# Performance work log

Measured on AMD Instinct MI355X. Metric: run time of the kernel, lower is better.

## Reference

```python
import jax, jax.numpy as jnp
import numpy as np

PERMS = ((0, 1, 2, 3), (2, 1, 3, 0), (3, 1, 0, 2))


def setup_inputs() -> dict:
    key = jax.random.key(0)
    ks = jax.random.split(key, 10)
    N_n1, F = 50000, 128
    N_imp = 100000
    H = 512
    h = jax.random.normal(ks[0], (N_n1, F), dtype=jnp.float32)
    idx = jax.random.randint(ks[1], (N_imp, 4), 0, N_n1, dtype=jnp.int64)
    s = 0.05
    W1 = jax.random.normal(ks[2], (4 * F, H), dtype=jnp.float32) * s
    b1 = jax.random.normal(ks[3], (H,), dtype=jnp.float32) * s
    W2 = jax.random.normal(ks[4], (H, H), dtype=jnp.float32) * s
    b2 = jax.random.normal(ks[5], (H,), dtype=jnp.float32) * s
    W3 = jax.random.normal(ks[6], (H, H), dtype=jnp.float32) * s
    b3 = jax.random.normal(ks[7], (H,), dtype=jnp.float32) * s
    Wo = jax.random.normal(ks[8], (H, 2), dtype=jnp.float32) * s
    bo = jax.random.normal(ks[9], (2,), dtype=jnp.float32) * s
    return {"h": h, "idx": idx, "W1": W1, "b1": b1, "W2": W2, "b2": b2,
            "W3": W3, "b3": b3, "Wo": Wo, "bo": bo}


def reference(h, idx, W1, b1, W2, b2, W3, b3, Wo, bo):
    # Message passing: copy_u + mean over exactly one edge per relation == gather.
    hi = h[idx]  # [N, 4, F]
    N = hi.shape[0]
    # Stack the 3 permutations of the 4 neighbor features: [3, N, 4F]
    x = jnp.stack([hi[:, jnp.array(p), :].reshape(N, -1) for p in PERMS], axis=0)
    # Shared MLP (config = [512, relu] x 3), broadcast over permutation axis.
    x = jax.nn.relu(x @ W1 + b1)
    x = jax.nn.relu(x @ W2 + b2)
    x = jax.nn.relu(x @ W3 + b3)
    pooled = jnp.sum(x, axis=0)  # Janossy sum over permutations: [N, 512]
    return pooled @ Wo + bo  # [N, 2]
```

## Files before the change

### kernel.cpp

```cpp
#include <hip/hip_runtime.h>
#include <stdint.h>
#include <stddef.h>


typedef __attribute__((ext_vector_type(8))) short short8;
typedef __attribute__((ext_vector_type(16))) float f32x16;
typedef __attribute__((ext_vector_type(4))) float floatv4;
typedef __attribute__((ext_vector_type(8))) unsigned short ushort8;

#define GLOAD_LDS16(g, l)                                                      \
  __builtin_amdgcn_global_load_lds(                                            \
      (const __attribute__((address_space(1))) void*)(g),                      \
      (__attribute__((address_space(3))) void*)(l), 16, 0, 0)

__device__ __forceinline__ unsigned short f2bf(float f) {
  unsigned int u = __float_as_uint(f);
  u += 0x7fffu + ((u >> 16) & 1u);
  return (unsigned short)(u >> 16);
}
__device__ __forceinline__ float bf2f(unsigned short s) {
  return __uint_as_float(((unsigned int)s) << 16);
}

#define NNODES 100000
#define MTOT   300000
#define HD     512
#define NH     50000
#define LSTR   152

__global__ __launch_bounds__(256) void prep_w(const float* __restrict__ W1,
                                              const float* __restrict__ W2,
                                              const float* __restrict__ W3,
                                              unsigned short* __restrict__ Wt) {
  int t = blockIdx.x * 256 + threadIdx.x;
  int layer = t >> 18;
  int r = t & 262143;
  int e = r & 7;
  int q16 = r >> 3;
  int s = q16 & 1023;
  int blk = q16 >> 10;
  int nb = blk >> 3, kt = blk & 7;
  int c = ((s >> 8) << 1) | ((s >> 5) & 1);
  int row = ((s >> 6) & 3) * 32 + (s & 31);
  int n = nb * 128 + row;
  int k = kt * 64 + c * 8 + e;
  const float* W = layer == 0 ? W1 : (layer == 1 ? W2 : W3);
  Wt[t] = f2bf(W[k * 512 + n]);
}

__global__ __launch_bounds__(256) void prep_hb(const float* __restrict__ h,
                                               unsigned short* __restrict__ hb) {
  int t = blockIdx.x * 256 + threadIdx.x;
  int v = t >> 4, c8 = (t & 15) * 8;
  const floatv4* hp = (const floatv4*)(h + (size_t)v * 128 + c8);
  floatv4 f0 = hp[0], f1 = hp[1];
  ushort8 o;
#pragma unroll
  for (int e = 0; e < 4; ++e) {
    o[e] = f2bf(f0[e]);
    o[4 + e] = f2bf(f1[e]);
  }
  *(ushort8*)(hb + (size_t)v * 128 + c8) = o;
}

__global__ __launch_bounds__(256) void init_out(float* __restrict__ out,
                                                const float* __restrict__ bo) {
  int t = blockIdx.x * 256 + threadIdx.x;
  if (t < 2 * NNODES) out[t] = bo[t & 1];
}

template <int GATHER, int FINAL>
__global__ __launch_bounds__(256, 4) void gemm_k(
    const unsigned short* __restrict__ A,
    const int* __restrict__ idx,
    const unsigned short* __restrict__ Wt,
    const float* __restrict__ bias,
    unsigned short* __restrict__ Xout,
    float* __restrict__ out, const float* __restrict__ Wo,
    int mchunk0) {
  __shared__ __align__(16) char smem[39936];
  char* sB = smem;
  char* sA = smem + 16384;
  int* sIdx = (int*)(smem + 32768);
  float* sWo = (float*)(smem + 38912);

  const int t = threadIdx.x;
  int bx = blockIdx.x;
  int xcd = bx & 7, tq = bx >> 3;
  int cbk = tq & 3;
  int rb = xcd + ((tq >> 2) << 3);
  int n0 = cbk * 128;
  int rb8 = rb * 8;
  int w = t >> 6, l = t & 63;
  int wmq = (w >> 1) * 2, wnq = (w & 1) * 2;
  int m32 = l & 31, half = l >> 5;
  int wm = wmq * 32;

  if (GATHER) {
    if (t < 128) {
      int m = mchunk0 + rb * 128 + t;
      unsigned um = (unsigned)m;
      unsigned n = um / 3u;
      int p = (int)(um - n * 3u);
      if (n >= NNODES) n = 0;
      const unsigned pk0 = 0x320u, pk1 = 0x111u, pk2 = 0x032u, pk3 = 0x203u;
      int sh = p * 4;
      sIdx[t * 4 + 0] = idx[n * 4 + ((pk0 >> sh) & 0xFu)];
      sIdx[t * 4 + 1] = idx[n * 4 + ((pk1 >> sh) & 0xFu)];
      sIdx[t * 4 + 2] = idx[n * 4 + ((pk2 >> sh) & 0xFu)];
      sIdx[t * 4 + 3] = idx[n * 4 + ((pk3 >> sh) & 0xFu)];
    }
    __syncthreads();
  }

  f32x16 acc[2][2];
#pragma unroll
  for (int i = 0; i < 2; ++i)
#pragma unroll
    for (int j = 0; j < 2; ++j)
#pragma unroll
      for (int r = 0; r < 16; ++r) acc[i][j][r] = 0.f;

  for (int kt = 0; kt < 8; ++kt) {
    short8 afr[4][2];
    if (!GATHER) {
      const unsigned short* ga = A + ((size_t)(rb8 + kt) * 1024) * 8;
#pragma unroll
      for (int ks = 0; ks < 4; ++ks)
#pragma unroll
        for (int i = 0; i < 2; ++i)
          afr[ks][i] = *(const short8*)(ga +
              (size_t)(ks * 256 + (wmq + i) * 64 + l) * 8);
    }
    {
      const unsigned short* gb = Wt + ((size_t)(cbk * 8 + kt) * 1024 + t) * 8;
#pragma unroll
      for (int i = 0; i < 4; ++i)
        GLOAD_LDS16(gb + (size_t)i * 2048, sB + (i * 256 + t) * 16);
    }
    if (GATHER) {
      int jblk = kt >> 1;
      int inner = (kt & 1) * 64;
#pragma unroll
      for (int i = 0; i < 4; ++i) {
        int s = i * 256 + t;
        int r = s >> 3;
        int cl = (s & 7) ^ (r & 7);
        int src = sIdx[r * 4 + jblk];
        GLOAD_LDS16(A + (size_t)src * 128 + inner + cl * 8, sA + s * 16);
      }
    }
    __syncthreads();
#pragma unroll
    for (int ks = 0; ks < 4; ++ks) {
      short8 bfr[2];
#pragma unroll
      for (int j = 0; j < 2; ++j)
        bfr[j] = *(const short8*)(sB + (ks * 256 + (wnq + j) * 64 + l) * 16);
      if (GATHER) {
        short8 ag[2];
        int cbp = ((ks << 1) + half) ^ (m32 & 7);
#pragma unroll
        for (int i = 0; i < 2; ++i)
          ag[i] = *(const short8*)(sA + (wm + i * 32 + m32) * 128 + cbp * 16);
#pragma unroll
        for (int i = 0; i < 2; ++i)
#pragma unroll
          for (int j = 0; j < 2; ++j)
            acc[i][j] = __builtin_amdgcn_mfma_f32_32x32x16_bf16(
                ag[i], bfr[j], acc[i][j], 0, 0, 0);
      } else {
#pragma unroll
        for (int i = 0; i < 2; ++i)
#pragma unroll
          for (int j = 0; j < 2; ++j)
            acc[i][j] = __builtin_amdgcn_mfma_f32_32x32x16_bf16(
                afr[ks][i], bfr[j], acc[i][j], 0, 0, 0);
      }
    }
    __syncthreads();
  }

  unsigned short* L = (unsigned short*)smem;
  if (FINAL && t < 256) sWo[t] = Wo[n0 * 2 + t];
#pragma unroll
  for (int i = 0; i < 2; ++i)
#pragma unroll
    for (int j = 0; j < 2; ++j) {
      int coll = wnq * 32 + j * 32 + m32;
      float bv = bias[n0 + coll];
#pragma unroll
      for (int r = 0; r < 16; ++r) {
        int rowl = wm + i * 32 + (r & 3) + 8 * (r >> 2) + 4 * half;
        float v = fmaxf(acc[i][j][r] + bv, 0.f);
        L[rowl * LSTR + coll] = f2bf(v);
      }
    }
  __syncthreads();

  if (!FINAL) {
#pragma unroll
    for (int v = 0; v < 8; ++v) {
      int chunk = v * 256 + t;
      int ktsel = chunk >> 10;
      int s = chunk & 1023;
      int ks_l = s >> 8;
      int rowhi = (s >> 6) & 3;
      int hb_ = (s >> 5) & 1;
      int row = rowhi * 32 + (s & 31);
      int col_local = ktsel * 64 + (((ks_l << 1) | hb_) << 3);
      ushort8 val = *(const ushort8*)(L + row * LSTR + col_local);
      *(ushort8*)(Xout + ((size_t)(rb8 + 2 * cbk + ktsel) * 1024 + s) * 8) = val;
    }
  } else {
    int r2 = t >> 1, jo = t & 1;
    int grow = mchunk0 + rb * 128 + r2;
    if (grow < MTOT) {
      const unsigned short* Lr = L + r2 * LSTR;
      float s = 0.f;
#pragma unroll
      for (int cc = 0; cc < 128; cc += 2) {
        unsigned int pair = *(const unsigned int*)(Lr + cc);
        s += bf2f((unsigned short)(pair & 0xffffu)) * sWo[2 * cc + jo];
        s += bf2f((unsigned short)(pair >> 16)) * sWo[2 * cc + 2 + jo];
      }
      int node = grow / 3;
      atomicAdd(out + node * 2 + jo, s);
    }
  }
}

extern "C" void kernel_launch(void* const* d_in, const int* in_sizes, int n_in,
                              void* d_out, int out_size, void* d_ws,
                              size_t ws_size, hipStream_t stream) {
  const float* h  = (const float*)d_in[0];
  const int*   ix = (const int*)d_in[1];
  const float* W1 = (const float*)d_in[2];
  const float* b1 = (const float*)d_in[3];
  const float* W2 = (const float*)d_in[4];
  const float* b2 = (const float*)d_in[5];
  const float* W3 = (const float*)d_in[6];
  const float* b3 = (const float*)d_in[7];
  const float* Wo = (const float*)d_in[8];
  const float* bo = (const float*)d_in[9];
  float* out = (float*)d_out;

  unsigned short* ws = (unsigned short*)d_ws;
  unsigned short* Wt = ws;
  unsigned short* hb = Wt + 786432;
  unsigned short* bufs = hb + 6400000;
  const size_t baseBytes = (786432ull + 6400000ull) * 2;

  size_t avail = ws_size > baseBytes ? ws_size - baseBytes : 0;
  size_t ncap = avail / (2ull * 3 * HD * sizeof(unsigned short));
  size_t nc = (ncap / 2048) * 2048;
  if (nc > 32768) nc = 32768;
  if (nc == 0) nc = 2048;
  unsigned short* X1 = bufs;
  unsigned short* X2 = X1 + nc * 3 * HD;

  prep_w<<<3072, 256, 0, stream>>>(W1, W2, W3, Wt);
  prep_hb<<<NH * 16 / 256, 256, 0, stream>>>(h, hb);
  init_out<<<(2 * NNODES + 255) / 256, 256, 0, stream>>>(out, bo);

  for (size_t n0c = 0; n0c < NNODES; n0c += nc) {
    size_t remn = (size_t)NNODES - n0c;
    size_t ncp = remn < nc ? ((remn + 2047) / 2048) * 2048 : nc;
    int rows = (int)(ncp * 3);
    int RB = rows / 128;
    int m0 = (int)(3 * n0c);
    gemm_k<1, 0><<<RB * 4, 256, 0, stream>>>(hb, ix, Wt, b1, X1, nullptr,
                                             nullptr, m0);
    gemm_k<0, 0><<<RB * 4, 256, 0, stream>>>(X1, nullptr, Wt + 262144, b2, X2,
                                             nullptr, nullptr, m0);
    gemm_k<0, 1><<<RB * 4, 256, 0, stream>>>(X2, nullptr, Wt + 524288, b3,
                                             nullptr, out, Wo, m0);
  }
}
```

Before: 666.4 us.

## Use 256x256 tiles with double-buffered LDS pipeline and 16x16x32 MFMA

Each GEMM block now computes a 256x256 output tile with 512 threads, instead of a 128x128 tile with 256 threads. Both A and B tiles are staged into double-buffered LDS with XOR-swizzled async global-to-LDS loads. The loads for the next k-steps are interleaved with four MFMA phases, separated by explicit barriers and setprio. Weight and intermediate activation layouts are rewritten to match the new tiling, and the epilogue is widened. This raises arithmetic intensity and overlaps memory with compute, at the cost of about 138KB of LDS per block, which limits occupancy to one block per CU, and more complex synchronisation.

```diff
diff --git a/kernel.cpp b/kernel.cpp
--- a/kernel.cpp
+++ b/kernel.cpp
@@ -4,7 +4,6 @@
 
 
 typedef __attribute__((ext_vector_type(8))) short short8;
-typedef __attribute__((ext_vector_type(16))) float f32x16;
 typedef __attribute__((ext_vector_type(4))) float floatv4;
 typedef __attribute__((ext_vector_type(8))) unsigned short ushort8;
 
@@ -26,7 +25,7 @@
 #define MTOT   300000
 #define HD     512
 #define NH     50000
-#define LSTR   152
+#define LSTR   264
 
 __global__ __launch_bounds__(256) void prep_w(const float* __restrict__ W1,
                                               const float* __restrict__ W2,
@@ -36,14 +35,12 @@
   int layer = t >> 18;
   int r = t & 262143;
   int e = r & 7;
-  int q16 = r >> 3;
-  int s = q16 & 1023;
-  int blk = q16 >> 10;
-  int nb = blk >> 3, kt = blk & 7;
-  int c = ((s >> 8) << 1) | ((s >> 5) & 1);
-  int row = ((s >> 6) & 3) * 32 + (s & 31);
-  int n = nb * 128 + row;
-  int k = kt * 64 + c * 8 + e;
+  int g = (r >> 3) & 7;
+  int row = (r >> 6) & 255;
+  int cbkt = r >> 14;
+  int cb = cbkt >> 3, kt = cbkt & 7;
+  int n = cb * 256 + row;
+  int k = kt * 64 + g * 8 + e;
   const float* W = layer == 0 ? W1 : (layer == 1 ? W2 : W3);
   Wt[t] = f2bf(W[k * 512 + n]);
 }
@@ -69,8 +66,77 @@
   if (t < 2 * NNODES) out[t] = bo[t & 1];
 }
 
+
+#define BAR()                            \
+  __builtin_amdgcn_sched_barrier(0);     \
+  __builtin_amdgcn_s_barrier();          \
+  __builtin_amdgcn_sched_barrier(0)
+
+#define STAGE_A(kk, odd)                                                       \
+  {                                                                            \
+    char* db = smem + ((kk) & 1) * 32768;                                      \
+    _Pragma("unroll")                                                          \
+    for (int qq = 0; qq < 2; ++qq) {                                           \
+      int q = (odd) + qq * 2;                                                  \
+      int row = q * 64 + tr;                                                   \
+      const unsigned short* sp;                                                \
+      if (GATHER) {                                                            \
+        int srcn = sIdx[row * 4 + ((kk) >> 1)];                                \
+        sp = A + (size_t)srcn * 128 + ((kk) & 1) * 64 + sxg * 8;               \
+      } else {                                                                 \
+        sp = A + (((size_t)(rb * 8 + (kk)) * 256 + row) * 8 + sxg) * 8;        \
+      }                                                                        \
+      GLOAD_LDS16(sp, db + q * 8192 + t * 16);                                 \
+    }                                                                          \
+  }
+
+#define STAGE_B(kk, odd)                                                       \
+  {                                                                            \
+    char* db = smem + 65536 + ((kk) & 1) * 32768;                              \
+    _Pragma("unroll")                                                          \
+    for (int qq = 0; qq < 2; ++qq) {                                           \
+      int q = (odd) + qq * 2;                                                  \
+      const unsigned short* sp =                                               \
+          Wt + (((size_t)(cb * 8 + (kk)) * 256 + q * 64 + tr) * 8 + sxg) * 8;  \
+      GLOAD_LDS16(sp, db + q * 8192 + t * 16);                                 \
+    }                                                                          \
+  }
+
+#define LDA(mh)                                                                \
+  _Pragma("unroll")                                                            \
+  for (int mi = 0; mi < 4; ++mi) {                                             \
+    const char* rbase = bA + (wmbase + (mh) * 64 + mi * 16 + lr) * 128;        \
+    a[mi][0] = *(const short8*)(rbase + xb0);                                  \
+    a[mi][1] = *(const short8*)(rbase + xb1);                                  \
+  }
+
+#define LDB(nh)                                                                \
+  _Pragma("unroll")                                                            \
+  for (int nj = 0; nj < 2; ++nj) {                                             \
+    const char* rbase = bB + (wnbase + (nh) * 32 + nj * 16 + lr) * 128;        \
+    b[(nh) * 2 + nj][0] = *(const short8*)(rbase + xb0);                       \
+    b[(nh) * 2 + nj][1] = *(const short8*)(rbase + xb1);                       \
+  }
+
+#define MMA(mh, nh)                                                            \
+  __builtin_amdgcn_s_setprio(1);                                               \
+  _Pragma("unroll")                                                            \
+  for (int mi = 0; mi < 4; ++mi)                                               \
+    _Pragma("unroll")                                                          \
+    for (int nj = 0; nj < 2; ++nj) {                                           \
+      acc[(mh) * 4 + mi][(nh) * 2 + nj] =                                      \
+          __builtin_amdgcn_mfma_f32_16x16x32_bf16(                             \
+              a[mi][0], b[(nh) * 2 + nj][0],                                   \
+              acc[(mh) * 4 + mi][(nh) * 2 + nj], 0, 0, 0);                     \
+      acc[(mh) * 4 + mi][(nh) * 2 + nj] =                                      \
+          __builtin_amdgcn_mfma_f32_16x16x32_bf16(                             \
+              a[mi][1], b[(nh) * 2 + nj][1],                                   \
+              acc[(mh) * 4 + mi][(nh) * 2 + nj], 0, 0, 0);                     \
+    }                                                                          \
+  __builtin_amdgcn_s_setprio(0);
+
 template <int GATHER, int FINAL>
-__global__ __launch_bounds__(256, 4) void gemm_k(
+__global__ __launch_bounds__(512, 2) void gemm_k(
     const unsigned short* __restrict__ A,
     const int* __restrict__ idx,
     const unsigned short* __restrict__ Wt,
@@ -78,31 +144,36 @@
     unsigned short* __restrict__ Xout,
     float* __restrict__ out, const float* __restrict__ Wo,
     int mchunk0) {
-  __shared__ __align__(16) char smem[39936];
-  char* sB = smem;
-  char* sA = smem + 16384;
-  int* sIdx = (int*)(smem + 32768);
-  float* sWo = (float*)(smem + 38912);
+  __shared__ __align__(16) char smem[141312];
+  int* sIdx = (int*)(smem + 135168);
+  float* sWo = (float*)(smem + 139264);
 
   const int t = threadIdx.x;
   int bx = blockIdx.x;
-  int xcd = bx & 7, tq = bx >> 3;
-  int cbk = tq & 3;
-  int rb = xcd + ((tq >> 2) << 3);
-  int n0 = cbk * 128;
-  int rb8 = rb * 8;
-  int w = t >> 6, l = t & 63;
-  int wmq = (w >> 1) * 2, wnq = (w & 1) * 2;
-  int m32 = l & 31, half = l >> 5;
-  int wm = wmq * 32;
-
+  int cpx = (int)gridDim.x >> 3;
+  int wg = (bx & 7) * cpx + (bx >> 3);
+  int cb = wg & 1;
+  int rb = wg >> 1;
+  int n0 = cb * 256;
+
+  const int l = t & 63;
+  const int w = t >> 6;
+  const int wmbase = (w >> 2) * 128;
+  const int wnbase = (w & 3) * 64;
+  const int lr = l & 15, lk = l >> 4;
+  const int xb0 = (lk ^ (lr & 7)) * 16;
+  const int xb1 = xb0 ^ 64;
+  const int tr = t >> 3;
+  const int sxg = (t & 7) ^ (tr & 7);
+
+  if (FINAL) sWo[t] = Wo[n0 * 2 + t];
   if (GATHER) {
-    if (t < 128) {
-      int m = mchunk0 + rb * 128 + t;
+    if (t < 256) {
+      int m = mchunk0 + rb * 256 + t;
       unsigned um = (unsigned)m;
       unsigned n = um / 3u;
       int p = (int)(um - n * 3u);
-      if (n >= NNODES) n = 0;
+      if (n >= (unsigned)NNODES) n = 0;
       const unsigned pk0 = 0x320u, pk1 = 0x111u, pk2 = 0x032u, pk3 = 0x203u;
       int sh = p * 4;
       sIdx[t * 4 + 0] = idx[n * 4 + ((pk0 >> sh) & 0xFu)];
@@ -113,113 +184,91 @@
     __syncthreads();
   }
 
-  f32x16 acc[2][2];
-#pragma unroll
-  for (int i = 0; i < 2; ++i)
-#pragma unroll
-    for (int j = 0; j < 2; ++j)
-#pragma unroll
-      for (int r = 0; r < 16; ++r) acc[i][j][r] = 0.f;
-
-  for (int kt = 0; kt < 8; ++kt) {
-    short8 afr[4][2];
-    if (!GATHER) {
-      const unsigned short* ga = A + ((size_t)(rb8 + kt) * 1024) * 8;
-#pragma unroll
-      for (int ks = 0; ks < 4; ++ks)
-#pragma unroll
-        for (int i = 0; i < 2; ++i)
-          afr[ks][i] = *(const short8*)(ga +
-              (size_t)(ks * 256 + (wmq + i) * 64 + l) * 8);
+  floatv4 acc[8][4];
+#pragma unroll
+  for (int i = 0; i < 8; ++i)
+#pragma unroll
+    for (int j = 0; j < 4; ++j)
+#pragma unroll
+      for (int r = 0; r < 4; ++r) acc[i][j][r] = 0.f;
+
+  STAGE_A(0, 0); STAGE_A(0, 1); STAGE_B(0, 0); STAGE_B(0, 1);
+  STAGE_A(1, 0); STAGE_B(1, 0); STAGE_B(1, 1);
+  asm volatile("s_waitcnt vmcnt(6)" ::: "memory");
+  BAR();
+
+#pragma unroll 2
+  for (int k = 0; k < 8; ++k) {
+    const char* bA = smem + (k & 1) * 32768;
+    const char* bB = smem + 65536 + (k & 1) * 32768;
+    short8 a[4][2], b[4][2];
+    LDA(0);
+    LDB(0);
+    if (k < 7) STAGE_A(k + 1, 1);
+    BAR();
+    MMA(0, 0);
+    BAR();
+    LDB(1);
+    if (k < 6) STAGE_A(k + 2, 0);
+    BAR();
+    MMA(0, 1);
+    BAR();
+    LDA(1);
+    if (k < 6) STAGE_B(k + 2, 0);
+    BAR();
+    MMA(1, 0);
+    BAR();
+    if (k < 6) STAGE_B(k + 2, 1);
+    BAR();
+    MMA(1, 1);
+    if (k < 6) {
+      asm volatile("s_waitcnt vmcnt(6)" ::: "memory");
+    } else {
+      asm volatile("s_waitcnt vmcnt(0)" ::: "memory");
     }
-    {
-      const unsigned short* gb = Wt + ((size_t)(cbk * 8 + kt) * 1024 + t) * 8;
-#pragma unroll
-      for (int i = 0; i < 4; ++i)
-        GLOAD_LDS16(gb + (size_t)i * 2048, sB + (i * 256 + t) * 16);
-    }
-    if (GATHER) {
-      int jblk = kt >> 1;
-      int inner = (kt & 1) * 64;
-#pragma unroll
-      for (int i = 0; i < 4; ++i) {
-        int s = i * 256 + t;
-        int r = s >> 3;
-        int cl = (s & 7) ^ (r & 7);
-        int src = sIdx[r * 4 + jblk];
-        GLOAD_LDS16(A + (size_t)src * 128 + inner + cl * 8, sA + s * 16);
+    BAR();
+  }
+
+  unsigned short* L = (unsigned short*)smem;
+  {
+    float bv[4];
+#pragma unroll
+    for (int nj = 0; nj < 4; ++nj) bv[nj] = bias[n0 + wnbase + nj * 16 + lr];
+#pragma unroll
+    for (int mi = 0; mi < 8; ++mi)
+#pragma unroll
+      for (int nj = 0; nj < 4; ++nj) {
+        int col = wnbase + nj * 16 + lr;
+#pragma unroll
+        for (int r = 0; r < 4; ++r) {
+          int row = wmbase + mi * 16 + lk * 4 + r;
+          float v = fmaxf(acc[mi][nj][r] + bv[nj], 0.f);
+          L[row * LSTR + col] = f2bf(v);
+        }
       }
-    }
-    __syncthreads();
-#pragma unroll
-    for (int ks = 0; ks < 4; ++ks) {
-      short8 bfr[2];
-#pragma unroll
-      for (int j = 0; j < 2; ++j)
-        bfr[j] = *(const short8*)(sB + (ks * 256 + (wnq + j) * 64 + l) * 16);
-      if (GATHER) {
-        short8 ag[2];
-        int cbp = ((ks << 1) + half) ^ (m32 & 7);
-#pragma unroll
-        for (int i = 0; i < 2; ++i)
-          ag[i] = *(const short8*)(sA + (wm + i * 32 + m32) * 128 + cbp * 16);
-#pragma unroll
-        for (int i = 0; i < 2; ++i)
-#pragma unroll
-          for (int j = 0; j < 2; ++j)
-            acc[i][j] = __builtin_amdgcn_mfma_f32_32x32x16_bf16(
-                ag[i], bfr[j], acc[i][j], 0, 0, 0);
-      } else {
-#pragma unroll
-        for (int i = 0; i < 2; ++i)
-#pragma unroll
-          for (int j = 0; j < 2; ++j)
-            acc[i][j] = __builtin_amdgcn_mfma_f32_32x32x16_bf16(
-                afr[ks][i], bfr[j], acc[i][j], 0, 0, 0);
-      }
-    }
-    __syncthreads();
-  }
-
-  unsigned short* L = (unsigned short*)smem;
-  if (FINAL && t < 256) sWo[t] = Wo[n0 * 2 + t];
-#pragma unroll
-  for (int i = 0; i < 2; ++i)
-#pragma unroll
-    for (int j = 0; j < 2; ++j) {
-      int coll = wnq * 32 + j * 32 + m32;
-      float bv = bias[n0 + coll];
-#pragma unroll
-      for (int r = 0; r < 16; ++r) {
-        int rowl = wm + i * 32 + (r & 3) + 8 * (r >> 2) + 4 * half;
-        float v = fmaxf(acc[i][j][r] + bv, 0.f);
-        L[rowl * LSTR + coll] = f2bf(v);
-      }
-    }
+  }
   __syncthreads();
 
   if (!FINAL) {
 #pragma unroll
-    for (int v = 0; v < 8; ++v) {
-      int chunk = v * 256 + t;
-      int ktsel = chunk >> 10;
-      int s = chunk & 1023;
-      int ks_l = s >> 8;
-      int rowhi = (s >> 6) & 3;
-      int hb_ = (s >> 5) & 1;
-      int row = rowhi * 32 + (s & 31);
-      int col_local = ktsel * 64 + (((ks_l << 1) | hb_) << 3);
-      ushort8 val = *(const ushort8*)(L + row * LSTR + col_local);
-      *(ushort8*)(Xout + ((size_t)(rb8 + 2 * cbk + ktsel) * 1024 + s) * 8) = val;
+    for (int it = 0; it < 16; ++it) {
+      int slot = it * 512 + t;
+      int ktq = slot >> 11;
+      int s = slot & 2047;
+      int row = s >> 3, g = s & 7;
+      ushort8 val = *(const ushort8*)(L + row * LSTR + ktq * 64 + g * 8);
+      *(ushort8*)(Xout +
+                  ((size_t)((rb * 8 + cb * 4 + ktq) * 256 + row) * 8 + g) * 8) =
+          val;
     }
   } else {
     int r2 = t >> 1, jo = t & 1;
-    int grow = mchunk0 + rb * 128 + r2;
+    int grow = mchunk0 + rb * 256 + r2;
     if (grow < MTOT) {
       const unsigned short* Lr = L + r2 * LSTR;
       float s = 0.f;
 #pragma unroll
-      for (int cc = 0; cc < 128; cc += 2) {
+      for (int cc = 0; cc < 256; cc += 2) {
         unsigned int pair = *(const unsigned int*)(Lr + cc);
         s += bf2f((unsigned short)(pair & 0xffffu)) * sWo[2 * cc + jo];
         s += bf2f((unsigned short)(pair >> 16)) * sWo[2 * cc + 2 + jo];
@@ -267,13 +316,13 @@
     size_t remn = (size_t)NNODES - n0c;
     size_t ncp = remn < nc ? ((remn + 2047) / 2048) * 2048 : nc;
     int rows = (int)(ncp * 3);
-    int RB = rows / 128;
+    int RB = rows / 256;
     int m0 = (int)(3 * n0c);
-    gemm_k<1, 0><<<RB * 4, 256, 0, stream>>>(hb, ix, Wt, b1, X1, nullptr,
+    gemm_k<1, 0><<<RB * 2, 512, 0, stream>>>(hb, ix, Wt, b1, X1, nullptr,
                                              nullptr, m0);
-    gemm_k<0, 0><<<RB * 4, 256, 0, stream>>>(X1, nullptr, Wt + 262144, b2, X2,
+    gemm_k<0, 0><<<RB * 2, 512, 0, stream>>>(X1, nullptr, Wt + 262144, b2, X2,
                                              nullptr, nullptr, m0);
-    gemm_k<0, 1><<<RB * 4, 256, 0, stream>>>(X2, nullptr, Wt + 524288, b3,
+    gemm_k<0, 1><<<RB * 2, 512, 0, stream>>>(X2, nullptr, Wt + 524288, b3,
                                              nullptr, out, Wo, m0);
   }
 }
```

After: 750.7 us. 12.7% more time.

## Split gather GEMM from dense GEMMs and double M-tile for dense layers

Applied to the files above, without the earlier changes.

Separates the gather-based first layer into its own kernel and gives layers 2 and 3 a new kernel with 256-row M tiles (4x2 MFMA tiles per wave), halving the number of blocks that reload each weight tile. The intermediate activation layout is changed to 256-row blocks so each wave loads its A fragments directly from global memory. The larger tile raises register pressure (launch bounds lowered to 2 blocks per SM) and the epilogue is done in two halves through a smaller LDS buffer, with extra barriers.

```diff
diff --git a/kernel.cpp b/kernel.cpp
--- a/kernel.cpp
+++ b/kernel.cpp
@@ -27,6 +27,7 @@
 #define HD     512
 #define NH     50000
 #define LSTR   152
+#define LSTR2  136
 
 __global__ __launch_bounds__(256) void prep_w(const float* __restrict__ W1,
                                               const float* __restrict__ W2,
@@ -69,20 +70,18 @@
   if (t < 2 * NNODES) out[t] = bo[t & 1];
 }
 
-template <int GATHER, int FINAL>
-__global__ __launch_bounds__(256, 4) void gemm_k(
+
+__global__ __launch_bounds__(256, 4) void gemm_g(
     const unsigned short* __restrict__ A,
     const int* __restrict__ idx,
     const unsigned short* __restrict__ Wt,
     const float* __restrict__ bias,
     unsigned short* __restrict__ Xout,
-    float* __restrict__ out, const float* __restrict__ Wo,
     int mchunk0) {
   __shared__ __align__(16) char smem[39936];
   char* sB = smem;
   char* sA = smem + 16384;
   int* sIdx = (int*)(smem + 32768);
-  float* sWo = (float*)(smem + 38912);
 
   const int t = threadIdx.x;
   int bx = blockIdx.x;
@@ -90,28 +89,25 @@
   int cbk = tq & 3;
   int rb = xcd + ((tq >> 2) << 3);
   int n0 = cbk * 128;
-  int rb8 = rb * 8;
   int w = t >> 6, l = t & 63;
   int wmq = (w >> 1) * 2, wnq = (w & 1) * 2;
   int m32 = l & 31, half = l >> 5;
   int wm = wmq * 32;
 
-  if (GATHER) {
-    if (t < 128) {
-      int m = mchunk0 + rb * 128 + t;
-      unsigned um = (unsigned)m;
-      unsigned n = um / 3u;
-      int p = (int)(um - n * 3u);
-      if (n >= NNODES) n = 0;
-      const unsigned pk0 = 0x320u, pk1 = 0x111u, pk2 = 0x032u, pk3 = 0x203u;
-      int sh = p * 4;
-      sIdx[t * 4 + 0] = idx[n * 4 + ((pk0 >> sh) & 0xFu)];
-      sIdx[t * 4 + 1] = idx[n * 4 + ((pk1 >> sh) & 0xFu)];
-      sIdx[t * 4 + 2] = idx[n * 4 + ((pk2 >> sh) & 0xFu)];
-      sIdx[t * 4 + 3] = idx[n * 4 + ((pk3 >> sh) & 0xFu)];
-    }
-    __syncthreads();
-  }
+  if (t < 128) {
+    int m = mchunk0 + rb * 128 + t;
+    unsigned um = (unsigned)m;
+    unsigned n = um / 3u;
+    int p = (int)(um - n * 3u);
+    if (n >= NNODES) n = 0;
+    const unsigned pk0 = 0x320u, pk1 = 0x111u, pk2 = 0x032u, pk3 = 0x203u;
+    int sh = p * 4;
+    sIdx[t * 4 + 0] = idx[n * 4 + ((pk0 >> sh) & 0xFu)];
+    sIdx[t * 4 + 1] = idx[n * 4 + ((pk1 >> sh) & 0xFu)];
+    sIdx[t * 4 + 2] = idx[n * 4 + ((pk2 >> sh) & 0xFu)];
+    sIdx[t * 4 + 3] = idx[n * 4 + ((pk3 >> sh) & 0xFu)];
+  }
+  __syncthreads();
 
   f32x16 acc[2][2];
 #pragma unroll
@@ -122,23 +118,13 @@
       for (int r = 0; r < 16; ++r) acc[i][j][r] = 0.f;
 
   for (int kt = 0; kt < 8; ++kt) {
-    short8 afr[4][2];
-    if (!GATHER) {
-      const unsigned short* ga = A + ((size_t)(rb8 + kt) * 1024) * 8;
-#pragma unroll
-      for (int ks = 0; ks < 4; ++ks)
-#pragma unroll
-        for (int i = 0; i < 2; ++i)
-          afr[ks][i] = *(const short8*)(ga +
-              (size_t)(ks * 256 + (wmq + i) * 64 + l) * 8);
-    }
     {
       const unsigned short* gb = Wt + ((size_t)(cbk * 8 + kt) * 1024 + t) * 8;
 #pragma unroll
       for (int i = 0; i < 4; ++i)
         GLOAD_LDS16(gb + (size_t)i * 2048, sB + (i * 256 + t) * 16);
     }
-    if (GATHER) {
+    {
       int jblk = kt >> 1;
       int inner = (kt & 1) * 64;
 #pragma unroll
@@ -157,32 +143,22 @@
 #pragma unroll
       for (int j = 0; j < 2; ++j)
         bfr[j] = *(const short8*)(sB + (ks * 256 + (wnq + j) * 64 + l) * 16);
-      if (GATHER) {
-        short8 ag[2];
-        int cbp = ((ks << 1) + half) ^ (m32 & 7);
-#pragma unroll
-        for (int i = 0; i < 2; ++i)
-          ag[i] = *(const short8*)(sA + (wm + i * 32 + m32) * 128 + cbp * 16);
-#pragma unroll
-        for (int i = 0; i < 2; ++i)
-#pragma unroll
-          for (int j = 0; j < 2; ++j)
-            acc[i][j] = __builtin_amdgcn_mfma_f32_32x32x16_bf16(
-                ag[i], bfr[j], acc[i][j], 0, 0, 0);
-      } else {
-#pragma unroll
-        for (int i = 0; i < 2; ++i)
-#pragma unroll
-          for (int j = 0; j < 2; ++j)
-            acc[i][j] = __builtin_amdgcn_mfma_f32_32x32x16_bf16(
-                afr[ks][i], bfr[j], acc[i][j], 0, 0, 0);
-      }
+      short8 ag[2];
+      int cbp = ((ks << 1) + half) ^ (m32 & 7);
+#pragma unroll
+      for (int i = 0; i < 2; ++i)
+        ag[i] = *(const short8*)(sA + (wm + i * 32 + m32) * 128 + cbp * 16);
+#pragma unroll
+      for (int i = 0; i < 2; ++i)
+#pragma unroll
+        for (int j = 0; j < 2; ++j)
+          acc[i][j] = __builtin_amdgcn_mfma_f32_32x32x16_bf16(
+              ag[i], bfr[j], acc[i][j], 0, 0, 0);
     }
     __syncthreads();
   }
 
   unsigned short* L = (unsigned short*)smem;
-  if (FINAL && t < 256) sWo[t] = Wo[n0 * 2 + t];
 #pragma unroll
   for (int i = 0; i < 2; ++i)
 #pragma unroll
@@ -198,35 +174,135 @@
     }
   __syncthreads();
 
-  if (!FINAL) {
-#pragma unroll
-    for (int v = 0; v < 8; ++v) {
-      int chunk = v * 256 + t;
-      int ktsel = chunk >> 10;
-      int s = chunk & 1023;
-      int ks_l = s >> 8;
-      int rowhi = (s >> 6) & 3;
-      int hb_ = (s >> 5) & 1;
-      int row = rowhi * 32 + (s & 31);
-      int col_local = ktsel * 64 + (((ks_l << 1) | hb_) << 3);
-      ushort8 val = *(const ushort8*)(L + row * LSTR + col_local);
-      *(ushort8*)(Xout + ((size_t)(rb8 + 2 * cbk + ktsel) * 1024 + s) * 8) = val;
-    }
-  } else {
-    int r2 = t >> 1, jo = t & 1;
-    int grow = mchunk0 + rb * 128 + r2;
-    if (grow < MTOT) {
-      const unsigned short* Lr = L + r2 * LSTR;
-      float s = 0.f;
-#pragma unroll
-      for (int cc = 0; cc < 128; cc += 2) {
-        unsigned int pair = *(const unsigned int*)(Lr + cc);
-        s += bf2f((unsigned short)(pair & 0xffffu)) * sWo[2 * cc + jo];
-        s += bf2f((unsigned short)(pair >> 16)) * sWo[2 * cc + 2 + jo];
+  int mblk = rb >> 1, rhalf = (rb & 1) * 4;
+#pragma unroll
+  for (int it = 0; it < 8; ++it) {
+    int c = it * 256 + t;
+    int ktl = c >> 10;
+    int s = c & 1023;
+    int ks = s >> 8, rg = (s >> 6) & 3, hf = (s >> 5) & 1, m = s & 31;
+    ushort8 val =
+        *(const ushort8*)(L + (rg * 32 + m) * LSTR + ktl * 64 + (ks * 2 + hf) * 8);
+    *(ushort8*)(Xout + ((size_t)((mblk * 8 + cbk * 2 + ktl) * 2048) + ks * 512 +
+                        (rhalf + rg) * 64 + hf * 32 + m) * 8) = val;
+  }
+}
+
+template <int FINAL>
+__global__ __launch_bounds__(256, 2) void gemm_d(
+    const unsigned short* __restrict__ A,
+    const unsigned short* __restrict__ Wt,
+    const float* __restrict__ bias,
+    unsigned short* __restrict__ Xout,
+    float* __restrict__ out, const float* __restrict__ Wo,
+    int mchunk0) {
+  __shared__ __align__(16) char smem[36864];
+  char* sB = smem;
+  float* sWo = (float*)(smem + 35840);
+
+  const int t = threadIdx.x;
+  int bx = blockIdx.x;
+  int xcd = bx & 7, tq = bx >> 3;
+  int cbk = tq & 3;
+  int rb = xcd + ((tq >> 2) << 3);
+  int n0 = cbk * 128;
+  int w = t >> 6, l = t & 63;
+  int wr = w >> 1, wc = w & 1;
+  int wm32 = wr * 4;
+  int m32 = l & 31, half = l >> 5;
+
+  if (FINAL) sWo[t] = Wo[n0 * 2 + t];
+
+  f32x16 acc[4][2];
+#pragma unroll
+  for (int i = 0; i < 4; ++i)
+#pragma unroll
+    for (int j = 0; j < 2; ++j)
+#pragma unroll
+      for (int r = 0; r < 16; ++r) acc[i][j][r] = 0.f;
+
+  for (int kt = 0; kt < 8; ++kt) {
+    short8 afr[4][4];
+    const unsigned short* ga = A + (size_t)(rb * 8 + kt) * 16384;
+#pragma unroll
+    for (int ks = 0; ks < 4; ++ks)
+#pragma unroll
+      for (int mi = 0; mi < 4; ++mi)
+        afr[ks][mi] = *(const short8*)(ga +
+            (size_t)(ks * 512 + (wm32 + mi) * 64 + l) * 8);
+    {
+      const unsigned short* gb = Wt + ((size_t)(cbk * 8 + kt) * 1024 + t) * 8;
+#pragma unroll
+      for (int i = 0; i < 4; ++i)
+        GLOAD_LDS16(gb + (size_t)i * 2048, sB + (i * 256 + t) * 16);
+    }
+    __syncthreads();
+#pragma unroll
+    for (int ks = 0; ks < 4; ++ks) {
+      short8 bfr[2];
+#pragma unroll
+      for (int j = 0; j < 2; ++j)
+        bfr[j] = *(const short8*)(sB + (ks * 256 + (wc * 2 + j) * 64 + l) * 16);
+#pragma unroll
+      for (int mi = 0; mi < 4; ++mi)
+#pragma unroll
+        for (int j = 0; j < 2; ++j)
+          acc[mi][j] = __builtin_amdgcn_mfma_f32_32x32x16_bf16(
+              afr[ks][mi], bfr[j], acc[mi][j], 0, 0, 0);
+    }
+    __syncthreads();
+  }
+
+  unsigned short* L = (unsigned short*)smem;
+#pragma unroll
+  for (int h = 0; h < 2; ++h) {
+    if (wr == h) {
+#pragma unroll
+      for (int mi = 0; mi < 4; ++mi)
+#pragma unroll
+        for (int j = 0; j < 2; ++j) {
+          int coll = wc * 64 + j * 32 + m32;
+          float bv = bias[n0 + coll];
+#pragma unroll
+          for (int r = 0; r < 16; ++r) {
+            int rowl = mi * 32 + (r & 3) + 8 * (r >> 2) + 4 * half;
+            float v = fmaxf(acc[mi][j][r] + bv, 0.f);
+            L[rowl * LSTR2 + coll] = f2bf(v);
+          }
+        }
+    }
+    __syncthreads();
+    if (!FINAL) {
+#pragma unroll
+      for (int it = 0; it < 8; ++it) {
+        int c = it * 256 + t;
+        int ktl = c >> 10;
+        int s = c & 1023;
+        int ks = s >> 8, rg = (s >> 6) & 3, hf = (s >> 5) & 1, m = s & 31;
+        ushort8 val = *(const ushort8*)(L + (rg * 32 + m) * LSTR2 + ktl * 64 +
+                                        (ks * 2 + hf) * 8);
+        *(ushort8*)(Xout + ((size_t)((rb * 8 + cbk * 2 + ktl) * 2048) +
+                            ks * 512 + (h * 4 + rg) * 64 + hf * 32 + m) * 8) =
+            val;
       }
-      int node = grow / 3;
-      atomicAdd(out + node * 2 + jo, s);
-    }
+    } else {
+      int r2 = t >> 1, jo = t & 1;
+      int grow = mchunk0 + rb * 256 + h * 128 + r2;
+      if (grow < MTOT) {
+        const unsigned short* Lr = L + r2 * LSTR2;
+        float sacc = 0.f;
+#pragma unroll
+        for (int cq = 0; cq < 16; ++cq) {
+          ushort8 pv = *(const ushort8*)(Lr + cq * 8);
+#pragma unroll
+          for (int e = 0; e < 8; ++e)
+            sacc += bf2f(pv[e]) * sWo[(cq * 8 + e) * 2 + jo];
+        }
+        int node = grow / 3;
+        atomicAdd(out + node * 2 + jo, sacc);
+      }
+    }
+    __syncthreads();
   }
 }
 
@@ -267,13 +343,13 @@
     size_t remn = (size_t)NNODES - n0c;
     size_t ncp = remn < nc ? ((remn + 2047) / 2048) * 2048 : nc;
     int rows = (int)(ncp * 3);
-    int RB = rows / 128;
+    int RBg = rows / 128;
+    int RBd = rows / 256;
     int m0 = (int)(3 * n0c);
-    gemm_k<1, 0><<<RB * 4, 256, 0, stream>>>(hb, ix, Wt, b1, X1, nullptr,
-                                             nullptr, m0);
-    gemm_k<0, 0><<<RB * 4, 256, 0, stream>>>(X1, nullptr, Wt + 262144, b2, X2,
-                                             nullptr, nullptr, m0);
-    gemm_k<0, 1><<<RB * 4, 256, 0, stream>>>(X2, nullptr, Wt + 524288, b3,
-                                             nullptr, out, Wo, m0);
-  }
-}
+    gemm_g<<<RBg * 4, 256, 0, stream>>>(hb, ix, Wt, b1, X1, m0);
+    gemm_d<0><<<RBd * 4, 256, 0, stream>>>(X1, Wt + 262144, b2, X2,
+                                           nullptr, nullptr, 0);
+    gemm_d<1><<<RBd * 4, 256, 0, stream>>>(X2, Wt + 524288, b3, nullptr,
+                                           out, Wo, m0);
+  }
+}
```

Measured after the change: 749.8 us. 1.13x slower.
